# Kernel tuning notes

Hardware: AMD Instinct MI355X
Metric: run time of the kernel (lower is better)

## Reference

```python
import jax, jax.numpy as jnp
import numpy as np
from jax import lax

H = W = 16   # grid_size
C = 64       # d_model
NH = 4       # attention heads
DH = C // NH
L = 2        # transformer layers
FF = 2048    # torch TransformerEncoderLayer default dim_feedforward
B = 8192
FEAT = 55


def _feats(pi, pj, gi, gj, wall):
    # pi,pj,gi,gj: scalar int32; wall: [H,W] float32
    f = jnp.float32
    ain = 2.0 * pi.astype(f) / (H - 1) - 1.0
    ajn = 2.0 * pj.astype(f) / (W - 1) - 1.0
    gin = 2.0 * gi.astype(f) / (H - 1) - 1.0
    gjn = 2.0 * gj.astype(f) / (W - 1) - 1.0
    dxg = gjn - ajn
    dyg = gin - ain
    dg = jnp.sqrt(dxg * dxg + dyg * dyg + 1e-8)
    goal = jnp.stack([ain, ajn, gin, gjn, dxg, dyg, dg, dyg / dg, dxg / dg])
    # first (up to) 3 wall locations in row-major order
    flat = wall.reshape(-1)
    idx = jnp.arange(H * W, dtype=jnp.int32)
    masked = jnp.where(flat == 1, idx, H * W)
    top3 = -lax.top_k(-masked, 3)[0]            # 3 smallest flat indices
    is_valid = top3 < H * W
    valid = is_valid.astype(f)
    safe = jnp.where(is_valid, top3, 0)
    win = 2.0 * (safe // W).astype(f) / (H - 1) - 1.0   # [3]
    wjn = 2.0 * (safe % W).astype(f) / (W - 1) - 1.0

    def rel(rin, rjn):
        dx = wjn - rjn
        dy = win - rin
        d = jnp.sqrt(dx * dx + dy * dy + 1e-8)
        return jnp.stack([win, wjn, dx, dy, d, dy / d, dx / d], axis=1)  # [3,7]

    aw = (rel(ain, ajn) * valid[:, None]).reshape(21)
    gw = (rel(gin, gjn) * valid[:, None]).reshape(21)
    up = jnp.where(pi > 0, wall[jnp.clip(pi - 1, 0, H - 1), pj], 1.0)
    dn = jnp.where(pi < H - 1, wall[jnp.clip(pi + 1, 0, H - 1), pj], 1.0)
    lf = jnp.where(pj > 0, wall[pi, jnp.clip(pj - 1, 0, W - 1)], 1.0)
    rt = jnp.where(pj < W - 1, wall[pi, jnp.clip(pj + 1, 0, W - 1)], 1.0)
    neigh = jnp.stack([up, dn, lf, rt])
    return jnp.concatenate([goal, aw, gw, neigh])  # [55]


def _ln(x, g, b):
    m = x.mean(-1, keepdims=True)
    v = ((x - m) ** 2).mean(-1, keepdims=True)
    return (x - m) / jnp.sqrt(v + 1e-5) * g + b


def _mha(x, wqkv, bqkv, wo, bo):
    # x: [B,T,C]
    qkv = x @ wqkv.T + bqkv               # [B,T,3C]
    q, k, v = jnp.split(qkv, 3, axis=-1)
    hds = lambda t: t.reshape(t.shape[0], t.shape[1], NH, DH).transpose(0, 2, 1, 3)
    q, k, v = hds(q), hds(k), hds(v)
    a = jax.nn.softmax(jnp.einsum('bhqd,bhkd->bhqk', q, k) / np.sqrt(DH).astype(np.float32), axis=-1)
    o = jnp.einsum('bhqk,bhkd->bhqd', a, v).transpose(0, 2, 1, 3).reshape(x.shape)
    return o @ wo.T + bo


def _forward(ai, aj, gi, gj, walls,
             mlp_w1, mlp_b1, mlp_w2, mlp_b2,
             in_proj_w, in_proj_b, out_w, out_b,
             ln1_g, ln1_b, ln2_g, ln2_b,
             ffn_w1, ffn_b1, ffn_w2, ffn_b2):
    wf = walls.astype(jnp.float32)
    # 5 positions per obs: current + 4 hypothetical moves (stay in place if off-grid)
    moves = jnp.array([[0, 0], [-1, 0], [1, 0], [0, -1], [0, 1]], dtype=jnp.int32)
    ni = ai[:, None] + moves[None, :, 0]
    nj = aj[:, None] + moves[None, :, 1]
    inb = (ni >= 0) & (ni < H) & (nj >= 0) & (nj < W)
    pi = jnp.where(inb, ni, ai[:, None])   # [B,5]
    pj = jnp.where(inb, nj, aj[:, None])
    per_obs = jax.vmap(_feats, in_axes=(0, 0, None, None, None))
    feats = jax.vmap(per_obs, in_axes=(0, 0, 0, 0, 0))(pi, pj, gi, gj, wf)  # [B,5,55]
    # feat_mlp: Linear -> GELU(exact) -> Linear
    tok = jax.nn.gelu(feats @ mlp_w1.T + mlp_b1, approximate=False) @ mlp_w2.T + mlp_b2  # [B,5,C]
    x = tok
    for l in range(L):
        x = _ln(x + _mha(x, in_proj_w[l], in_proj_b[l], out_w[l], out_b[l]), ln1_g[l], ln1_b[l])
        hdn = jax.nn.relu(x @ ffn_w1[l].T + ffn_b1[l]) @ ffn_w2[l].T + ffn_b2[l]
        x = _ln(x + hdn, ln2_g[l], ln2_b[l])
    return x  # [B,5,C]


def setup_inputs() -> dict:
    key = jax.random.key(0)
    ks = jax.random.split(key, 24)
    s = 0.02
    inp = {
        'ai': jax.random.randint(ks[0], (B,), 0, H, dtype=jnp.int32),
        'aj': jax.random.randint(ks[1], (B,), 0, W, dtype=jnp.int32),
        'gi': jax.random.randint(ks[2], (B,), 0, H, dtype=jnp.int32),
        'gj': jax.random.randint(ks[3], (B,), 0, W, dtype=jnp.int32),
        'walls': jax.random.randint(ks[4], (B, H, W), 0, 2, dtype=jnp.int32),
        'mlp_w1': jax.random.normal(ks[5], (128, FEAT)) * s,
        'mlp_b1': jnp.zeros((128,)),
        'mlp_w2': jax.random.normal(ks[6], (C, 128)) * s,
        'mlp_b2': jnp.zeros((C,)),
        'in_proj_w': jax.random.normal(ks[7], (L, 3 * C, C)) * s,
        'in_proj_b': jnp.zeros((L, 3 * C)),
        'out_w': jax.random.normal(ks[8], (L, C, C)) * s,
        'out_b': jnp.zeros((L, C)),
        'ln1_g': jnp.ones((L, C)),
        'ln1_b': jnp.zeros((L, C)),
        'ln2_g': jnp.ones((L, C)),
        'ln2_b': jnp.zeros((L, C)),
        'ffn_w1': jax.random.normal(ks[9], (L, FF, C)) * s,
        'ffn_b1': jnp.zeros((L, FF)),
        'ffn_w2': jax.random.normal(ks[10], (L, C, FF)) * s,
        'ffn_b2': jnp.zeros((L, C)),
    }
    return inp


def reference(ai, aj, gi, gj, walls,
              mlp_w1, mlp_b1, mlp_w2, mlp_b2,
              in_proj_w, in_proj_b, out_w, out_b,
              ln1_g, ln1_b, ln2_g, ln2_b,
              ffn_w1, ffn_b1, ffn_w2, ffn_b2):
    return _forward(ai, aj, gi, gj, walls,
                    mlp_w1, mlp_b1, mlp_w2, mlp_b2,
                    in_proj_w, in_proj_b, out_w, out_b,
                    ln1_g, ln1_b, ln2_g, ln2_b,
                    ffn_w1, ffn_b1, ffn_w2, ffn_b2)
```

## Files before the change

kernel.cpp:

```cpp
#include <hip/hip_runtime.h>
#include <math.h>

#define NT 256

typedef __attribute__((ext_vector_type(4))) float  f32x4;
typedef __attribute__((ext_vector_type(8))) short  bf16x8;
typedef __attribute__((ext_vector_type(4))) short  bf16x4;

static __device__ __forceinline__ short f2bf(float f) {
    unsigned u = __builtin_bit_cast(unsigned, f);
    unsigned r = (u + 0x7fffu + ((u >> 16) & 1u)) >> 16;
    return (short)r;
}

static __device__ __forceinline__ unsigned pk2(float a, float b) {
    unsigned ua = __builtin_bit_cast(unsigned, a);
    unsigned ub = __builtin_bit_cast(unsigned, b);
    ua = (ua + 0x7fffu + ((ua >> 16) & 1u)) >> 16;
    ub = (ub + 0x7fffu + ((ub >> 16) & 1u)) & 0xffff0000u;
    return ua | ub;
}
static __device__ __forceinline__ bf16x4 pk_bf16(f32x4 d) {
    uint2 t;
    t.x = pk2(d[0], d[1]);
    t.y = pk2(d[2], d[3]);
    return __builtin_bit_cast(bf16x4, t);
}
static __device__ __forceinline__ bf16x8 pk_bf16x8(f32x4 a, f32x4 b) {
    uint4 t;
    t.x = pk2(a[0], a[1]);
    t.y = pk2(a[2], a[3]);
    t.z = pk2(b[0], b[1]);
    t.w = pk2(b[2], b[3]);
    return __builtin_bit_cast(bf16x8, t);
}
static __device__ __forceinline__ bf16x4 lo4(bf16x8 v) {
    return __builtin_shufflevector(v, v, 0, 1, 2, 3);
}
static __device__ __forceinline__ bf16x4 hi4(bf16x8 v) {
    return __builtin_shufflevector(v, v, 4, 5, 6, 7);
}

#define MFMA16x32(a, b, c) __builtin_amdgcn_mfma_f32_16x16x32_bf16(a, b, c, 0, 0, 0)

#if __has_builtin(__builtin_amdgcn_mfma_f32_16x16x16bf16_1k)
static __device__ __forceinline__ f32x4 mfma16x16(bf16x4 a, bf16x4 b, f32x4 c) {
    return __builtin_amdgcn_mfma_f32_16x16x16bf16_1k(a, b, c, 0, 0, 0);
}
#elif __has_builtin(__builtin_amdgcn_mfma_f32_16x16x16_bf16)
static __device__ __forceinline__ f32x4 mfma16x16(bf16x4 a, bf16x4 b, f32x4 c) {
    return __builtin_amdgcn_mfma_f32_16x16x16_bf16(a, b, c, 0, 0, 0);
}
#else
static __device__ __forceinline__ f32x4 mfma16x16(bf16x4 a, bf16x4 b, f32x4 c) {
    f32x4 d;
    asm("v_mfma_f32_16x16x16_bf16 %0, %1, %2, %3" : "=v"(d) : "v"(a), "v"(b), "v"(c));
    return d;
}
#endif

#define WS_FPK  0
#define WS_QKV  524288
#define WS_WO   548864
#define WS_BASE 557056
#define WS_MW1  557056
#define WS_MW2  565248
#define WS_TOTAL 573440

__global__ __launch_bounds__(NT) void k_cvtw(
    const float* __restrict__ ffn_w1, const float* __restrict__ ffn_w2,
    const float* __restrict__ in_proj_w, const float* __restrict__ out_w,
    const float* __restrict__ mlp_w1, const float* __restrict__ mlp_w2,
    int do_mlp,
    unsigned short* __restrict__ ws)
{
    int i = blockIdx.x * NT + threadIdx.x;
    if (i < 524288) {
        int l = i >> 18;
        int w = i & 262143;
        int c = w >> 13;
        int ww = w & 8191;
        int region = ww >> 11;
        int q = ww & 2047;
        int lane = q >> 3, j = q & 7;
        int hc = lane >> 6, lg = (lane >> 4) & 3, lr = lane & 15;
        const float* W1 = ffn_w1 + l * 131072;
        const float* W2 = ffn_w2 + l * 131072;
        float v;
        if (region == 0)
            v = W1[(c * 64 + hc * 16 + lr) * 64 + lg * 8 + j];
        else if (region == 1)
            v = W1[(c * 64 + hc * 16 + lr) * 64 + 32 + lg * 8 + j];
        else {
            int nf = ((region - 2) << 1) + (j >> 2);
            int r = j & 3;
            v = W2[(nf * 16 + lr) * 2048 + c * 64 + hc * 16 + lg * 4 + r];
        }
        ws[WS_FPK + i] = (unsigned short)f2bf(v);
    }
    if (i < 24576) ws[WS_QKV + i] = (unsigned short)f2bf(in_proj_w[i]);
    if (i < 8192)  ws[WS_WO + i]  = (unsigned short)f2bf(out_w[i]);
    if (do_mlp && i < 8192) {
        int row = i >> 6, col = i & 63;
        ws[WS_MW1 + i] = (col < 55) ? (unsigned short)f2bf(mlp_w1[row * 55 + col]) : 0;
        ws[WS_MW2 + i] = (unsigned short)f2bf(mlp_w2[i]);
    }
}

#define FB 16
__global__ __launch_bounds__(320) void k_feat2(
    const int* __restrict__ ai, const int* __restrict__ aj,
    const int* __restrict__ gi, const int* __restrict__ gj,
    const int* __restrict__ walls,
    const unsigned short* __restrict__ w1p,
    const float* __restrict__ b1,
    const unsigned short* __restrict__ w2p,
    const float* __restrict__ b2,
    float* __restrict__ x)
{
    const int tid = threadIdx.x;
    const int ob0 = blockIdx.x * FB;
    __shared__ unsigned char wl[FB * 256];
    __shared__ short fe[80][72];
    __shared__ int t3s[FB][3];

    for (int i = tid; i < FB * 256; i += 320)
        wl[i] = (unsigned char)walls[ob0 * 256 + i];
    __syncthreads();

    const int lane = tid & 63;
    const int wid  = tid >> 6;

    if (wid < 4) {
        #pragma unroll
        for (int q = 0; q < 4; ++q) {
            const int o = wid * 4 + q;
            const unsigned char* wp = wl + o * 256 + lane * 4;
            int m = (wp[0] ? 1 : 0) | (wp[1] ? 2 : 0) | (wp[2] ? 4 : 0) | (wp[3] ? 8 : 0);
            unsigned long long bm[4];
            bm[0] = __ballot(m & 1); bm[1] = __ballot(m & 2);
            bm[2] = __ballot(m & 4); bm[3] = __ballot(m & 8);
            int res[3];
            #pragma unroll
            for (int c = 0; c < 3; ++c) {
                int best = 1 << 30, bj = -1;
                #pragma unroll
                for (int j = 0; j < 4; ++j)
                    if (bm[j]) {
                        int cand = 4 * (int)__builtin_ctzll(bm[j]) + j;
                        if (cand < best) { best = cand; bj = j; }
                    }
                res[c] = (bj >= 0) ? best : 256;
                if (bj >= 0) bm[bj] &= bm[bj] - 1;
            }
            if (lane == 0) {
                t3s[o][0] = res[0]; t3s[o][1] = res[1]; t3s[o][2] = res[2];
            }
        }
    }
    __syncthreads();

    if (tid < 80) {
        const int o = tid / 5, tq = tid % 5;
        const int gob = ob0 + o;
        const unsigned char* wp = wl + o * 256;
        const int mi[5] = {0, -1, 1, 0, 0};
        const int mj[5] = {0, 0, 0, -1, 1};
        const int a_i = ai[gob], a_j = aj[gob];
        int ni = a_i + mi[tq], nj = a_j + mj[tq];
        bool inb = (ni >= 0 && ni < 16 && nj >= 0 && nj < 16);
        int pi = inb ? ni : a_i;
        int pj = inb ? nj : a_j;

        float f[64];
        #pragma unroll
        for (int d = 55; d < 64; ++d) f[d] = 0.f;

        const float ain = 2.f * (float)pi / 15.f - 1.f;
        const float ajn = 2.f * (float)pj / 15.f - 1.f;
        const float gin = 2.f * (float)gi[gob] / 15.f - 1.f;
        const float gjn = 2.f * (float)gj[gob] / 15.f - 1.f;
        const float dxg = gjn - ajn, dyg = gin - ain;
        const float dg = sqrtf(dxg * dxg + dyg * dyg + 1e-8f);
        f[0] = ain; f[1] = ajn; f[2] = gin; f[3] = gjn;
        f[4] = dxg; f[5] = dyg; f[6] = dg; f[7] = dyg / dg; f[8] = dxg / dg;

        #pragma unroll
        for (int w = 0; w < 3; ++w) {
            int idx = t3s[o][w];
            float vm = (idx < 256) ? 1.f : 0.f;
            int safe = (idx < 256) ? idx : 0;
            float win = 2.f * (float)(safe >> 4) / 15.f - 1.f;
            float wjn = 2.f * (float)(safe & 15) / 15.f - 1.f;
            {
                float dx = wjn - ajn, dy = win - ain;
                float d = sqrtf(dx * dx + dy * dy + 1e-8f);
                f[9 + w * 7 + 0] = win * vm; f[9 + w * 7 + 1] = wjn * vm;
                f[9 + w * 7 + 2] = dx * vm;  f[9 + w * 7 + 3] = dy * vm;
                f[9 + w * 7 + 4] = d * vm;
                f[9 + w * 7 + 5] = (dy / d) * vm; f[9 + w * 7 + 6] = (dx / d) * vm;
            }
            {
                float dx = wjn - gjn, dy = win - gin;
                float d = sqrtf(dx * dx + dy * dy + 1e-8f);
                f[30 + w * 7 + 0] = win * vm; f[30 + w * 7 + 1] = wjn * vm;
                f[30 + w * 7 + 2] = dx * vm;  f[30 + w * 7 + 3] = dy * vm;
                f[30 + w * 7 + 4] = d * vm;
                f[30 + w * 7 + 5] = (dy / d) * vm; f[30 + w * 7 + 6] = (dx / d) * vm;
            }
        }
        f[51] = (pi > 0)  ? (float)wp[(pi - 1) * 16 + pj] : 1.f;
        f[52] = (pi < 15) ? (float)wp[(pi + 1) * 16 + pj] : 1.f;
        f[53] = (pj > 0)  ? (float)wp[pi * 16 + (pj - 1)] : 1.f;
        f[54] = (pj < 15) ? (float)wp[pi * 16 + (pj + 1)] : 1.f;

        unsigned* dst = (unsigned*)&fe[tid][0];
        #pragma unroll
        for (int d = 0; d < 32; ++d)
            dst[d] = pk2(f[2 * d], f[2 * d + 1]);
    }
    __syncthreads();

    const int lr = lane & 15;
    const int lg = lane >> 4;
    const int t0 = wid * 16;

    bf16x8 bf0 = *(const bf16x8*)&fe[t0 + lr][lg * 8];
    bf16x8 bf1 = *(const bf16x8*)&fe[t0 + lr][32 + lg * 8];

    f32x4 acc[4] = {};
    #pragma unroll
    for (int hc = 0; hc < 8; ++hc) {
        bf16x8 a0 = *(const bf16x8*)(w1p + (hc * 16 + lr) * 64 + lg * 8);
        bf16x8 a1 = *(const bf16x8*)(w1p + (hc * 16 + lr) * 64 + 32 + lg * 8);
        f32x4 d = {0.f, 0.f, 0.f, 0.f};
        d = MFMA16x32(a0, bf0, d);
        d = MFMA16x32(a1, bf1, d);
        f32x4 b1v = *(const f32x4*)(b1 + hc * 16 + lg * 4);
        bf16x4 h;
        #pragma unroll
        for (int r = 0; r < 4; ++r) {
            float s = d[r] + b1v[r];
            h[r] = f2bf(0.5f * s * (1.f + erff(s * 0.70710678118654752f)));
        }
        #pragma unroll
        for (int nf = 0; nf < 4; ++nf) {
            bf16x4 bw = *(const bf16x4*)(w2p + (nf * 16 + lr) * 128 + hc * 16 + lg * 4);
            acc[nf] = mfma16x16(h, bw, acc[nf]);
        }
    }

    const int gt0 = blockIdx.x * 80 + t0;
    #pragma unroll
    for (int r = 0; r < 4; ++r) {
        const int row = (gt0 + lg * 4 + r) * 64;
        #pragma unroll
        for (int nf = 0; nf < 4; ++nf)
            x[row + nf * 16 + lr] = acc[nf][r] + b2[nf * 16 + lr];
    }
}

__global__ __launch_bounds__(NT) void k_feat(
    const int* __restrict__ ai, const int* __restrict__ aj,
    const int* __restrict__ gi, const int* __restrict__ gj,
    const int* __restrict__ walls,
    const float* __restrict__ w1, const float* __restrict__ b1,
    const float* __restrict__ w2, const float* __restrict__ b2,
    float* __restrict__ xout)
{
    const int b = blockIdx.x;
    const int tid = threadIdx.x;
    __shared__ float wallf[256];
    __shared__ unsigned long long wmask[4];
    __shared__ int   t3[3];
    __shared__ float feats[5][55];
    __shared__ float h1[5][128];

    int wv = walls[b * 256 + tid];
    wallf[tid] = (float)wv;
    unsigned long long bm = __ballot(wv == 1);
    if ((tid & 63) == 0) wmask[tid >> 6] = bm;
    __syncthreads();

    if (tid == 0) {
        int c = 0;
        for (int w = 0; w < 4 && c < 3; ++w) {
            unsigned long long mm = wmask[w];
            while (mm && c < 3) {
                t3[c++] = w * 64 + __builtin_ctzll(mm);
                mm &= mm - 1;
            }
        }
        for (; c < 3; ++c) t3[c] = 256;
    }
    __syncthreads();

    if (tid < 5) {
        const int mi[5] = {0, -1, 1, 0, 0};
        const int mj[5] = {0, 0, 0, -1, 1};
        const int a_i = ai[b], a_j = aj[b];
        int ni = a_i + mi[tid], nj = a_j + mj[tid];
        bool inb = (ni >= 0 && ni < 16 && nj >= 0 && nj < 16);
        int pi = inb ? ni : a_i;
        int pj = inb ? nj : a_j;

        const float ain = 2.f * (float)pi / 15.f - 1.f;
        const float ajn = 2.f * (float)pj / 15.f - 1.f;
        const float gin = 2.f * (float)gi[b] / 15.f - 1.f;
        const float gjn = 2.f * (float)gj[b] / 15.f - 1.f;
        const float dxg = gjn - ajn, dyg = gin - ain;
        const float dg = sqrtf(dxg * dxg + dyg * dyg + 1e-8f);

        float* f = feats[tid];
        f[0] = ain; f[1] = ajn; f[2] = gin; f[3] = gjn;
        f[4] = dxg; f[5] = dyg; f[6] = dg; f[7] = dyg / dg; f[8] = dxg / dg;

        for (int w = 0; w < 3; ++w) {
            int idx = t3[w];
            float vm = (idx < 256) ? 1.f : 0.f;
            int safe = (idx < 256) ? idx : 0;
            float win = 2.f * (float)(safe >> 4) / 15.f - 1.f;
            float wjn = 2.f * (float)(safe & 15) / 15.f - 1.f;
            {
                float dx = wjn - ajn, dy = win - ain;
                float d = sqrtf(dx * dx + dy * dy + 1e-8f);
                float* o = f + 9 + w * 7;
                o[0] = win * vm; o[1] = wjn * vm; o[2] = dx * vm; o[3] = dy * vm;
                o[4] = d * vm;  o[5] = (dy / d) * vm; o[6] = (dx / d) * vm;
            }
            {
                float dx = wjn - gjn, dy = win - gin;
                float d = sqrtf(dx * dx + dy * dy + 1e-8f);
                float* o = f + 30 + w * 7;
                o[0] = win * vm; o[1] = wjn * vm; o[2] = dx * vm; o[3] = dy * vm;
                o[4] = d * vm;  o[5] = (dy / d) * vm; o[6] = (dx / d) * vm;
            }
        }
        f[51] = (pi > 0)  ? wallf[(pi - 1) * 16 + pj] : 1.f;
        f[52] = (pi < 15) ? wallf[(pi + 1) * 16 + pj] : 1.f;
        f[53] = (pj > 0)  ? wallf[pi * 16 + (pj - 1)] : 1.f;
        f[54] = (pj < 15) ? wallf[pi * 16 + (pj + 1)] : 1.f;
    }
    __syncthreads();

    for (int i = tid; i < 640; i += NT) {
        int p = i >> 7, j = i & 127;
        float s = b1[j];
        const float* wr = w1 + j * 55;
        const float* fp = feats[p];
        #pragma unroll
        for (int k = 0; k < 55; ++k) s += fp[k] * wr[k];
        h1[p][j] = 0.5f * s * (1.f + erff(s * 0.70710678118654752f));
    }
    __syncthreads();

    for (int i = tid; i < 320; i += NT) {
        int p = i >> 6, j = i & 63;
        float s = b2[j];
        const float* wr = w2 + j * 128;
        #pragma unroll
        for (int k = 0; k < 128; ++k) s += h1[p][k] * wr[k];
        xout[b * 320 + i] = s;
    }
}

__global__ __launch_bounds__(128) void k_att2(
    float* __restrict__ x,
    const unsigned short* __restrict__ wqkv,
    const float* __restrict__ bqkv,
    const unsigned short* __restrict__ wo,
    const float* __restrict__ bo,
    const float* __restrict__ g1, const float* __restrict__ be1)
{
    const int lane = threadIdx.x & 63;
    const int wid  = threadIdx.x >> 6;
    const int lr = lane & 15;
    const int lg = lane >> 4;
    const int o0 = (blockIdx.x * 2 + wid) * 16;

    __shared__ unsigned short o_lds[2][5][16][68];

    bf16x8 bx[5][2];
    #pragma unroll
    for (int tq = 0; tq < 5; ++tq)
        #pragma unroll
        for (int kf = 0; kf < 2; ++kf) {
            const float* p = x + ((o0 + lr) * 5 + tq) * 64 + kf * 32 + lg * 8;
            bf16x8 v;
            #pragma unroll
            for (int j = 0; j < 8; ++j) v[j] = f2bf(p[j]);
            bx[tq][kf] = v;
        }

    for (int h = 0; h < 4; ++h) {
        bf16x8 aq[2], ak[2], av[2];
        #pragma unroll
        for (int kf = 0; kf < 2; ++kf) {
            aq[kf] = *(const bf16x8*)(wqkv + (h * 16 + lr) * 64 + kf * 32 + lg * 8);
            ak[kf] = *(const bf16x8*)(wqkv + (64 + h * 16 + lr) * 64 + kf * 32 + lg * 8);
            av[kf] = *(const bf16x8*)(wqkv + (128 + h * 16 + lr) * 64 + kf * 32 + lg * 8);
        }
        f32x4 bq = *(const f32x4*)(bqkv + h * 16 + lg * 4);
        f32x4 bk = *(const f32x4*)(bqkv + 64 + h * 16 + lg * 4);
        f32x4 bv = *(const f32x4*)(bqkv + 128 + h * 16 + lg * 4);

        f32x4 qf[5], kf_[5];
        #pragma unroll
        for (int t = 0; t < 5; ++t) {
            f32x4 d = {0.f, 0.f, 0.f, 0.f};
            d = MFMA16x32(aq[0], bx[t][0], d);
            d = MFMA16x32(aq[1], bx[t][1], d);
            qf[t] = d + bq;
            f32x4 e = {0.f, 0.f, 0.f, 0.f};
            e = MFMA16x32(ak[0], bx[t][0], e);
            e = MFMA16x32(ak[1], bx[t][1], e);
            kf_[t] = e + bk;
        }

        float p_[5][5];
        #pragma unroll
        for (int tq = 0; tq < 5; ++tq)
            #pragma unroll
            for (int tk = 0; tk < 5; ++tk) {
                float s = qf[tq][0] * kf_[tk][0] + qf[tq][1] * kf_[tk][1]
                        + qf[tq][2] * kf_[tk][2] + qf[tq][3] * kf_[tk][3];
                s += __shfl_xor(s, 16);
                s += __shfl_xor(s, 32);
                p_[tq][tk] = s * 0.25f;
            }
        #pragma unroll
        for (int tq = 0; tq < 5; ++tq) {
            float m = p_[tq][0];
            #pragma unroll
            for (int tk = 1; tk < 5; ++tk) m = fmaxf(m, p_[tq][tk]);
            float sum = 0.f;
            #pragma unroll
            for (int tk = 0; tk < 5; ++tk) {
                float e = __expf(p_[tq][tk] - m);
                p_[tq][tk] = e; sum += e;
            }
            float inv = 1.f / sum;
            #pragma unroll
            for (int tk = 0; tk < 5; ++tk) p_[tq][tk] *= inv;
        }

        f32x4 vf[5];
        #pragma unroll
        for (int t = 0; t < 5; ++t) {
            f32x4 d = {0.f, 0.f, 0.f, 0.f};
            d = MFMA16x32(av[0], bx[t][0], d);
            d = MFMA16x32(av[1], bx[t][1], d);
            vf[t] = d + bv;
        }

        #pragma unroll
        for (int tq = 0; tq < 5; ++tq) {
            f32x4 o = {0.f, 0.f, 0.f, 0.f};
            #pragma unroll
            for (int tk = 0; tk < 5; ++tk) o += p_[tq][tk] * vf[tk];
            bf16x4 pk = pk_bf16(o);
            *(bf16x4*)&o_lds[wid][tq][lr][h * 16 + lg * 4] = pk;
        }
    }

    f32x4 acc[5][4] = {};
    for (int h = 0; h < 4; ++h) {
        bf16x4 bwo[4];
        #pragma unroll
        for (int nt = 0; nt < 4; ++nt)
            bwo[nt] = *(const bf16x4*)(wo + (nt * 16 + lr) * 64 + h * 16 + lg * 4);
        #pragma unroll
        for (int tq = 0; tq < 5; ++tq) {
            bf16x4 a2 = *(const bf16x4*)&o_lds[wid][tq][lr][h * 16 + lg * 4];
            #pragma unroll
            for (int nt = 0; nt < 4; ++nt)
                acc[tq][nt] = mfma16x16(a2, bwo[nt], acc[tq][nt]);
        }
    }

    #pragma unroll
    for (int r = 0; r < 4; ++r) {
        const int obs = o0 + lg * 4 + r;
        #pragma unroll
        for (int tq = 0; tq < 5; ++tq) {
            const int row = (obs * 5 + tq) * 64;
            float y[4];
            float s = 0.f;
            #pragma unroll
            for (int nt = 0; nt < 4; ++nt) {
                int c = nt * 16 + lr;
                float v = acc[tq][nt][r] + bo[c] + x[row + c];
                y[nt] = v; s += v;
            }
            s += __shfl_xor(s, 1); s += __shfl_xor(s, 2);
            s += __shfl_xor(s, 4); s += __shfl_xor(s, 8);
            float mean = s * (1.f / 64.f);
            float q = 0.f;
            #pragma unroll
            for (int nt = 0; nt < 4; ++nt) { float d0 = y[nt] - mean; q += d0 * d0; }
            q += __shfl_xor(q, 1); q += __shfl_xor(q, 2);
            q += __shfl_xor(q, 4); q += __shfl_xor(q, 8);
            float rstd = rsqrtf(q * (1.f / 64.f) + 1e-5f);
            #pragma unroll
            for (int nt = 0; nt < 4; ++nt) {
                int c = nt * 16 + lr;
                x[row + c] = (y[nt] - mean) * rstd * g1[c] + be1[c];
            }
        }
    }
}

__global__ __launch_bounds__(NT) void k_att(
    float* __restrict__ x,
    const float* __restrict__ wqkv, const float* __restrict__ bqkv,
    const float* __restrict__ wo, const float* __restrict__ bo,
    const float* __restrict__ g1, const float* __restrict__ be1)
{
    const int b = blockIdx.x;
    const int tid = threadIdx.x;
    __shared__ float xs[5][64];
    __shared__ float qkv[5][192];
    __shared__ float att[4][5][5];
    __shared__ float os[5][64];
    __shared__ float xr[5][64];
    __shared__ float stat[5][2];

    for (int i = tid; i < 320; i += NT) xs[i >> 6][i & 63] = x[b * 320 + i];
    __syncthreads();

    for (int i = tid; i < 960; i += NT) {
        int p = i / 192, j = i % 192;
        float s = bqkv[j];
        const float* wr = wqkv + j * 64;
        const float* xm = xs[p];
        #pragma unroll
        for (int k = 0; k < 64; ++k) s += xm[k] * wr[k];
        qkv[p][j] = s;
    }
    __syncthreads();

    if (tid < 100) {
        int h = tid / 25, r = tid % 25, q = r / 5, kk = r % 5;
        float s = 0.f;
        #pragma unroll
        for (int d = 0; d < 16; ++d) s += qkv[q][h * 16 + d] * qkv[kk][64 + h * 16 + d];
        att[h][q][kk] = s * 0.25f;
    }
    __syncthreads();

    if (tid < 20) {
        int h = tid / 5, q = tid % 5;
        float m = att[h][q][0];
        for (int k = 1; k < 5; ++k) m = fmaxf(m, att[h][q][k]);
        float sum = 0.f;
        for (int k = 0; k < 5; ++k) { float e = expf(att[h][q][k] - m); att[h][q][k] = e; sum += e; }
        float inv = 1.f / sum;
        for (int k = 0; k < 5; ++k) att[h][q][k] *= inv;
    }
    __syncthreads();

    for (int i = tid; i < 320; i += NT) {
        int p = i >> 6, c = i & 63, h = c >> 4;
        float s = 0.f;
        #pragma unroll
        for (int k = 0; k < 5; ++k) s += att[h][p][k] * qkv[k][128 + c];
        os[p][c] = s;
    }
    __syncthreads();

    for (int i = tid; i < 320; i += NT) {
        int p = i >> 6, c = i & 63;
        float s = bo[c];
        const float* wr = wo + c * 64;
        const float* om = os[p];
        #pragma unroll
        for (int k = 0; k < 64; ++k) s += om[k] * wr[k];
        xr[p][c] = xs[p][c] + s;
    }
    __syncthreads();

    if (tid < 5) {
        float m = 0.f;
        for (int k = 0; k < 64; ++k) m += xr[tid][k];
        m *= (1.f / 64.f);
        float v = 0.f;
        for (int k = 0; k < 64; ++k) { float d = xr[tid][k] - m; v += d * d; }
        v *= (1.f / 64.f);
        stat[tid][0] = m;
        stat[tid][1] = 1.f / sqrtf(v + 1e-5f);
    }
    __syncthreads();

    for (int i = tid; i < 320; i += NT) {
        int p = i >> 6, c = i & 63;
        x[b * 320 + i] = (xr[p][c] - stat[p][0]) * stat[p][1] * g1[c] + be1[c];
    }
}

#define PKCH 8192
__global__ __launch_bounds__(256, 2) void k_ffn8(
    float* __restrict__ x,
    const unsigned short* __restrict__ wpk,
    const float* __restrict__ b1,
    const float* __restrict__ b2,
    const float* __restrict__ g2, const float* __restrict__ be2)
{
    __shared__ float red[4][4][4][64][4];
    const int tid  = threadIdx.x;
    const int lane = tid & 63;
    const int wid  = tid >> 6;
    const int lr = lane & 15;
    const int lg = lane >> 4;
    const int row0 = blockIdx.x * 64;

    bf16x8 bx[4][2];
    #pragma unroll
    for (int mf = 0; mf < 4; ++mf)
        #pragma unroll
        for (int kk = 0; kk < 2; ++kk) {
            const float* p = x + (row0 + mf * 16 + lr) * 64 + kk * 32 + lg * 8;
            f32x4 aa = *(const f32x4*)(p);
            f32x4 bb = *(const f32x4*)(p + 4);
            bx[mf][kk] = pk_bf16x8(aa, bb);
        }

    f32x4 acc[4][4] = {};
    const int fbase = (lg * 16 + lr) * 8;
    const unsigned short* wp = wpk + (wid * 8) * PKCH;
    const float* b1w = b1 + wid * 512;

    for (int c = 0; c < 8; ++c) {
        const unsigned short* L = wp + c * PKCH;
        bf16x8 rA[4], rB[4], rC[4], rD[4];
        #pragma unroll
        for (int hc = 0; hc < 4; ++hc) {
            rA[hc] = *(const bf16x8*)&L[hc * 512 + fbase];
            rB[hc] = *(const bf16x8*)&L[2048 + hc * 512 + fbase];
            rC[hc] = *(const bf16x8*)&L[4096 + hc * 512 + fbase];
            rD[hc] = *(const bf16x8*)&L[6144 + hc * 512 + fbase];
        }
        f32x4 b1v[4];
        #pragma unroll
        for (int hc = 0; hc < 4; ++hc)
            b1v[hc] = *(const f32x4*)(b1w + c * 64 + hc * 16 + lg * 4);

        #pragma unroll
        for (int hc = 0; hc < 4; ++hc) {
            #pragma unroll
            for (int mf = 0; mf < 4; ++mf) {
                f32x4 d = MFMA16x32(rA[hc], bx[mf][0], b1v[hc]);
                d = MFMA16x32(rB[hc], bx[mf][1], d);
                #pragma unroll
                for (int r = 0; r < 4; ++r) d[r] = fmaxf(d[r], 0.f);
                bf16x4 h = pk_bf16(d);
                acc[mf][0] = mfma16x16(h, lo4(rC[hc]), acc[mf][0]);
                acc[mf][1] = mfma16x16(h, hi4(rC[hc]), acc[mf][1]);
                acc[mf][2] = mfma16x16(h, lo4(rD[hc]), acc[mf][2]);
                acc[mf][3] = mfma16x16(h, hi4(rD[hc]), acc[mf][3]);
            }
        }
    }

    #pragma unroll
    for (int mf = 0; mf < 4; ++mf)
        #pragma unroll
        for (int nf = 0; nf < 4; ++nf)
            *(f32x4*)&red[wid][mf][nf][lane][0] = acc[mf][nf];
    __syncthreads();

    f32x4 vr[4];
    #pragma unroll
    for (int nf = 0; nf < 4; ++nf) {
        f32x4 s0 = *(const f32x4*)&red[0][wid][nf][lane][0];
        f32x4 s1 = *(const f32x4*)&red[1][wid][nf][lane][0];
        f32x4 s2 = *(const f32x4*)&red[2][wid][nf][lane][0];
        f32x4 s3 = *(const f32x4*)&red[3][wid][nf][lane][0];
        vr[nf] = (s0 + s1) + (s2 + s3);
    }

    #pragma unroll
    for (int r = 0; r < 4; ++r) {
        const int m = row0 + wid * 16 + lg * 4 + r;
        float v[4];
        float s = 0.f;
        #pragma unroll
        for (int nf = 0; nf < 4; ++nf) {
            int cc = nf * 16 + lr;
            float y = vr[nf][r] + b2[cc] + x[m * 64 + cc];
            v[nf] = y; s += y;
        }
        s += __shfl_xor(s, 1); s += __shfl_xor(s, 2);
        s += __shfl_xor(s, 4); s += __shfl_xor(s, 8);
        float mean = s * (1.f / 64.f);
        float q = 0.f;
        #pragma unroll
        for (int nf = 0; nf < 4; ++nf) { float d0 = v[nf] - mean; q += d0 * d0; }
        q += __shfl_xor(q, 1); q += __shfl_xor(q, 2);
        q += __shfl_xor(q, 4); q += __shfl_xor(q, 8);
        float rstd = rsqrtf(q * (1.f / 64.f) + 1e-5f);
        #pragma unroll
        for (int nf = 0; nf < 4; ++nf) {
            int cc = nf * 16 + lr;
            x[m * 64 + cc] = (v[nf] - mean) * rstd * g2[cc] + be2[cc];
        }
    }
}

#define GRP 8
#define ROWS (GRP * 5)
__global__ __launch_bounds__(NT) void k_ffn(
    float* __restrict__ x,
    const float* __restrict__ w1, const float* __restrict__ b1,
    const float* __restrict__ w2, const float* __restrict__ b2,
    const float* __restrict__ g2, const float* __restrict__ be2)
{
    const int tid = threadIdx.x;
    const int base = blockIdx.x * (ROWS * 64);
    __shared__ float xs[ROWS][64];
    __shared__ float hch[ROWS][128];
    __shared__ float stat[ROWS][2];

    for (int i = tid; i < ROWS * 64; i += NT) xs[i >> 6][i & 63] = x[base + i];
    __syncthreads();

    const int c = tid & 63;
    const int g = tid >> 6;
    float acc[10];
    #pragma unroll
    for (int r = 0; r < 10; ++r) acc[r] = 0.f;

    for (int ch = 0; ch < 16; ++ch) {
        for (int ii = tid; ii < ROWS * 128; ii += NT) {
            int m = ii >> 7, j = ii & 127;
            int jj = (ch << 7) + j;
            float s = b1[jj];
            const float* wr = w1 + jj * 64;
            const float* xm = xs[m];
            #pragma unroll
            for (int k = 0; k < 64; ++k) s += xm[k] * wr[k];
            hch[m][j] = fmaxf(s, 0.f);
        }
        __syncthreads();
        const float* w2r = w2 + c * 2048 + (ch << 7);
        for (int j = 0; j < 128; ++j) {
            float wv = w2r[j];
            #pragma unroll
            for (int r = 0; r < 10; ++r) acc[r] += hch[g * 10 + r][j] * wv;
        }
        __syncthreads();
    }

    #pragma unroll
    for (int r = 0; r < 10; ++r) {
        int m = g * 10 + r;
        hch[m][c] = acc[r] + b2[c] + xs[m][c];
    }
    __syncthreads();

    if (tid < ROWS) {
        float m = 0.f;
        for (int k = 0; k < 64; ++k) m += hch[tid][k];
        m *= (1.f / 64.f);
        float v = 0.f;
        for (int k = 0; k < 64; ++k) { float d = hch[tid][k] - m; v += d * d; }
        v *= (1.f / 64.f);
        stat[tid][0] = m;
        stat[tid][1] = 1.f / sqrtf(v + 1e-5f);
    }
    __syncthreads();

    for (int i = tid; i < ROWS * 64; i += NT) {
        int m = i >> 6, cc = i & 63;
        x[base + i] = (hch[m][cc] - stat[m][0]) * stat[m][1] * g2[cc] + be2[cc];
    }
}

extern "C" void kernel_launch(void* const* d_in, const int* in_sizes, int n_in,
                              void* d_out, int out_size, void* d_ws, size_t ws_size,
                              hipStream_t stream)
{
    (void)in_sizes; (void)n_in; (void)out_size;
    const int*   ai       = (const int*)d_in[0];
    const int*   aj       = (const int*)d_in[1];
    const int*   gi       = (const int*)d_in[2];
    const int*   gj       = (const int*)d_in[3];
    const int*   walls    = (const int*)d_in[4];
    const float* mlp_w1   = (const float*)d_in[5];
    const float* mlp_b1   = (const float*)d_in[6];
    const float* mlp_w2   = (const float*)d_in[7];
    const float* mlp_b2   = (const float*)d_in[8];
    const float* in_proj_w = (const float*)d_in[9];
    const float* in_proj_b = (const float*)d_in[10];
    const float* out_w    = (const float*)d_in[11];
    const float* out_b    = (const float*)d_in[12];
    const float* ln1_g    = (const float*)d_in[13];
    const float* ln1_b    = (const float*)d_in[14];
    const float* ln2_g    = (const float*)d_in[15];
    const float* ln2_b    = (const float*)d_in[16];
    const float* ffn_w1   = (const float*)d_in[17];
    const float* ffn_b1   = (const float*)d_in[18];
    const float* ffn_w2   = (const float*)d_in[19];
    const float* ffn_b2   = (const float*)d_in[20];

    float* x = (float*)d_out;
    const int B = 8192;
    const bool fast  = ws_size >= (size_t)(WS_BASE * 2);
    const bool fast2 = ws_size >= (size_t)(WS_TOTAL * 2);
    unsigned short* wsbf = (unsigned short*)d_ws;

    if (fast)
        k_cvtw<<<2048, NT, 0, stream>>>(ffn_w1, ffn_w2, in_proj_w, out_w,
                                        mlp_w1, mlp_w2, fast2 ? 1 : 0, wsbf);

    if (fast2) {
        k_feat2<<<B / FB, 320, 0, stream>>>(ai, aj, gi, gj, walls,
            wsbf + WS_MW1, mlp_b1, wsbf + WS_MW2, mlp_b2, x);
    } else {
        k_feat<<<B, NT, 0, stream>>>(ai, aj, gi, gj, walls,
                                     mlp_w1, mlp_b1, mlp_w2, mlp_b2, x);
    }

    for (int l = 0; l < 2; ++l) {
        if (fast) {
            k_att2<<<256, 128, 0, stream>>>(x,
                wsbf + WS_QKV + l * 12288, in_proj_b + l * 192,
                wsbf + WS_WO + l * 4096, out_b + l * 64,
                ln1_g + l * 64, ln1_b + l * 64);
            k_ffn8<<<640, 256, 0, stream>>>(x,
                wsbf + WS_FPK + l * 262144, ffn_b1 + l * 2048,
                ffn_b2 + l * 64,
                ln2_g + l * 64, ln2_b + l * 64);
        } else {
            k_att<<<B, NT, 0, stream>>>(x,
                in_proj_w + l * 192 * 64, in_proj_b + l * 192,
                out_w + l * 64 * 64, out_b + l * 64,
                ln1_g + l * 64, ln1_b + l * 64);
            k_ffn<<<B / GRP, NT, 0, stream>>>(x,
                ffn_w1 + l * 2048 * 64, ffn_b1 + l * 2048,
                ffn_w2 + l * 64 * 2048, ffn_b2 + l * 64,
                ln2_g + l * 64, ln2_b + l * 64);
        }
    }
}
```

Before: 168.1 us.

## Split attention heads across waves and stage out-projection and LayerNorm through LDS

The attention kernel is restructured so that each block handles 16 observations with 4 waves, one wave per head, instead of one wave looping over all 4 heads. The out-projection is then split by output column tile per wave. Residual sums are staged in shared memory, and LayerNorm is done with 16-lane groups using vectorized loads and stores. The input load now uses vector float4 reads packed to bf16. This quadruples the number of waves to expose more parallelism and shorten each wave's serial chain, at the cost of two block barriers and extra LDS traffic.

```diff
diff --git a/kernel.cpp b/kernel.cpp
--- a/kernel.cpp
+++ b/kernel.cpp
@@ -364,21 +364,23 @@
     }
 }
 
-__global__ __launch_bounds__(128) void k_att2(
-    float* __restrict__ x,
+__global__ __launch_bounds__(256, 2) void k_att3(
+    const float* __restrict__ x, float* __restrict__ xo,
     const unsigned short* __restrict__ wqkv,
     const float* __restrict__ bqkv,
     const unsigned short* __restrict__ wo,
     const float* __restrict__ bo,
     const float* __restrict__ g1, const float* __restrict__ be1)
 {
-    const int lane = threadIdx.x & 63;
-    const int wid  = threadIdx.x >> 6;
+    const int tid  = threadIdx.x;
+    const int lane = tid & 63;
+    const int wid  = tid >> 6;
     const int lr = lane & 15;
     const int lg = lane >> 4;
-    const int o0 = (blockIdx.x * 2 + wid) * 16;
-
-    __shared__ unsigned short o_lds[2][5][16][68];
+    const int o0 = blockIdx.x * 16;
+
+    __shared__ unsigned short o_sh[5][16][68];
+    __shared__ float          y_sh[5][16][68];
 
     bf16x8 bx[5][2];
     #pragma unroll
@@ -386,13 +388,13 @@
         #pragma unroll
         for (int kf = 0; kf < 2; ++kf) {
             const float* p = x + ((o0 + lr) * 5 + tq) * 64 + kf * 32 + lg * 8;
-            bf16x8 v;
-            #pragma unroll
-            for (int j = 0; j < 8; ++j) v[j] = f2bf(p[j]);
-            bx[tq][kf] = v;
-        }
-
-    for (int h = 0; h < 4; ++h) {
+            f32x4 aa = *(const f32x4*)(p);
+            f32x4 bb = *(const f32x4*)(p + 4);
+            bx[tq][kf] = pk_bf16x8(aa, bb);
+        }
+
+    {
+        const int h = wid;
         bf16x8 aq[2], ak[2], av[2];
         #pragma unroll
         for (int kf = 0; kf < 2; ++kf) {
@@ -404,7 +406,7 @@
         f32x4 bk = *(const f32x4*)(bqkv + 64 + h * 16 + lg * 4);
         f32x4 bv = *(const f32x4*)(bqkv + 128 + h * 16 + lg * 4);
 
-        f32x4 qf[5], kf_[5];
+        f32x4 qf[5], kf_[5], vf[5];
         #pragma unroll
         for (int t = 0; t < 5; ++t) {
             f32x4 d = {0.f, 0.f, 0.f, 0.f};
@@ -415,6 +417,10 @@
             e = MFMA16x32(ak[0], bx[t][0], e);
             e = MFMA16x32(ak[1], bx[t][1], e);
             kf_[t] = e + bk;
+            f32x4 g = {0.f, 0.f, 0.f, 0.f};
+            g = MFMA16x32(av[0], bx[t][0], g);
+            g = MFMA16x32(av[1], bx[t][1], g);
+            vf[t] = g + bv;
         }
 
         float p_[5][5];
@@ -444,67 +450,64 @@
             for (int tk = 0; tk < 5; ++tk) p_[tq][tk] *= inv;
         }
 
-        f32x4 vf[5];
-        #pragma unroll
-        for (int t = 0; t < 5; ++t) {
-            f32x4 d = {0.f, 0.f, 0.f, 0.f};
-            d = MFMA16x32(av[0], bx[t][0], d);
-            d = MFMA16x32(av[1], bx[t][1], d);
-            vf[t] = d + bv;
-        }
-
         #pragma unroll
         for (int tq = 0; tq < 5; ++tq) {
             f32x4 o = {0.f, 0.f, 0.f, 0.f};
             #pragma unroll
             for (int tk = 0; tk < 5; ++tk) o += p_[tq][tk] * vf[tk];
-            bf16x4 pk = pk_bf16(o);
-            *(bf16x4*)&o_lds[wid][tq][lr][h * 16 + lg * 4] = pk;
-        }
-    }
-
-    f32x4 acc[5][4] = {};
-    for (int h = 0; h < 4; ++h) {
+            *(bf16x4*)&o_sh[tq][lr][h * 16 + lg * 4] = pk_bf16(o);
+        }
+    }
+    __syncthreads();
+
+    {
         bf16x4 bwo[4];
         #pragma unroll
-        for (int nt = 0; nt < 4; ++nt)
-            bwo[nt] = *(const bf16x4*)(wo + (nt * 16 + lr) * 64 + h * 16 + lg * 4);
+        for (int kf = 0; kf < 4; ++kf)
+            bwo[kf] = *(const bf16x4*)(wo + (wid * 16 + lr) * 64 + kf * 16 + lg * 4);
+
         #pragma unroll
         for (int tq = 0; tq < 5; ++tq) {
-            bf16x4 a2 = *(const bf16x4*)&o_lds[wid][tq][lr][h * 16 + lg * 4];
-            #pragma unroll
-            for (int nt = 0; nt < 4; ++nt)
-                acc[tq][nt] = mfma16x16(a2, bwo[nt], acc[tq][nt]);
-        }
-    }
-
-    #pragma unroll
-    for (int r = 0; r < 4; ++r) {
-        const int obs = o0 + lg * 4 + r;
-        #pragma unroll
-        for (int tq = 0; tq < 5; ++tq) {
-            const int row = (obs * 5 + tq) * 64;
-            float y[4];
-            float s = 0.f;
-            #pragma unroll
-            for (int nt = 0; nt < 4; ++nt) {
-                int c = nt * 16 + lr;
-                float v = acc[tq][nt][r] + bo[c] + x[row + c];
-                y[nt] = v; s += v;
-            }
+            f32x4 acc = {0.f, 0.f, 0.f, 0.f};
+            #pragma unroll
+            for (int kf = 0; kf < 4; ++kf) {
+                bf16x4 a2 = *(const bf16x4*)&o_sh[tq][lr][kf * 16 + lg * 4];
+                acc = mfma16x16(a2, bwo[kf], acc);
+            }
+            const int col = wid * 16 + lr;
+            const float bv2 = bo[col];
+            #pragma unroll
+            for (int r = 0; r < 4; ++r) {
+                const int obs = lg * 4 + r;
+                y_sh[tq][obs][col] =
+                    acc[r] + bv2 + x[((o0 + obs) * 5 + tq) * 64 + col];
+            }
+        }
+    }
+    __syncthreads();
+
+    {
+        const int grp = tid >> 4;
+        const int l16 = tid & 15;
+        #pragma unroll
+        for (int it = 0; it < 5; ++it) {
+            const int tq = it, obs = grp;
+            f32x4 v = *(const f32x4*)&y_sh[tq][obs][l16 * 4];
+            float s = v[0] + v[1] + v[2] + v[3];
             s += __shfl_xor(s, 1); s += __shfl_xor(s, 2);
             s += __shfl_xor(s, 4); s += __shfl_xor(s, 8);
             float mean = s * (1.f / 64.f);
             float q = 0.f;
             #pragma unroll
-            for (int nt = 0; nt < 4; ++nt) { float d0 = y[nt] - mean; q += d0 * d0; }
+            for (int j = 0; j < 4; ++j) { float d0 = v[j] - mean; q += d0 * d0; }
             q += __shfl_xor(q, 1); q += __shfl_xor(q, 2);
             q += __shfl_xor(q, 4); q += __shfl_xor(q, 8);
             float rstd = rsqrtf(q * (1.f / 64.f) + 1e-5f);
-            #pragma unroll
-            for (int nt = 0; nt < 4; ++nt) {
-                int c = nt * 16 + lr;
-                x[row + c] = (y[nt] - mean) * rstd * g1[c] + be1[c];
+            const int row = ((o0 + obs) * 5 + tq) * 64;
+            #pragma unroll
+            for (int j = 0; j < 4; ++j) {
+                int c = l16 * 4 + j;
+                xo[row + c] = (v[j] - mean) * rstd * g1[c] + be1[c];
             }
         }
     }
@@ -822,7 +825,7 @@
 
     for (int l = 0; l < 2; ++l) {
         if (fast) {
-            k_att2<<<256, 128, 0, stream>>>(x,
+            k_att3<<<512, 256, 0, stream>>>(x, x,
                 wsbf + WS_QKV + l * 12288, in_proj_b + l * 192,
                 wsbf + WS_WO + l * 4096, out_b + l * 64,
                 ln1_g + l * 64, ln1_b + l * 64);
```

Result: faster. 149.1 us, median of 3 (-11.3%).
